# Kernel tuning notes

Hardware: AMD Instinct MI355X
Metric: run time of the kernel (lower is better)

The kernel has to match this reference:

```python
import jax, jax.numpy as jnp
import numpy as np

NUM_EMBEDDINGS = 1024
EMBEDDING_DIM = 256
COMMITMENT_COST = 0.25
DECAY = 0.99
EPS = 1e-05
BATCH = 65536


def setup_inputs() -> dict:
    key = jax.random.key(0)
    k1, k2 = jax.random.split(key, 2)
    z_e = jax.random.normal(k1, (BATCH, EMBEDDING_DIM), dtype=jnp.float32)
    embedding = jax.random.normal(k2, (NUM_EMBEDDINGS, EMBEDDING_DIM), dtype=jnp.float32)
    ema_cluster_size = jnp.zeros((NUM_EMBEDDINGS,), dtype=jnp.float32)
    ema_w = embedding  # buffer initialized as a clone of the codebook
    return {"z_e": z_e, "embedding": embedding,
            "ema_cluster_size": ema_cluster_size, "ema_w": ema_w}


def reference(z_e, embedding, ema_cluster_size, ema_w):
    B, D = z_e.shape
    K = embedding.shape[0]

    # Squared L2 distances: ||z||^2 + ||e||^2 - 2 z.e  -> [B, K]
    z_sq = jnp.sum(z_e * z_e, axis=1, keepdims=True)          # [B, 1]
    e_sq = jnp.sum(embedding * embedding, axis=1)[None, :]    # [1, K]
    ze = jnp.matmul(z_e, embedding.T)                         # [B, K]
    distances = z_sq + e_sq - 2.0 * ze

    encoding_indices = jnp.argmin(distances, axis=1)          # [B]

    # Gather instead of one-hot matmul (same math as encodings @ embedding)
    z_q = embedding[encoding_indices]                         # [B, D]
    z_q_st = z_e + jax.lax.stop_gradient(z_q - z_e)

    vq_loss = COMMITMENT_COST * jnp.mean(
        (jax.lax.stop_gradient(z_q) - z_e) ** 2)

    # EMA statistics (training-mode update); segment_sum == one-hot reductions
    cluster_size = jax.ops.segment_sum(
        jnp.ones((B,), dtype=z_e.dtype), encoding_indices, num_segments=K)
    new_ema_cluster_size = DECAY * ema_cluster_size + (1.0 - DECAY) * cluster_size
    dw = jax.ops.segment_sum(z_e, encoding_indices, num_segments=K)  # [K, D]
    new_ema_w = DECAY * ema_w + (1.0 - DECAY) * dw

    n = jnp.sum(new_ema_cluster_size)
    smoothed = (new_ema_cluster_size + EPS) / (n + K * EPS) * n
    new_embedding = new_ema_w / smoothed[:, None]

    avg_probs = cluster_size / B
    perplexity = jnp.exp(-jnp.sum(avg_probs * jnp.log(avg_probs + 1e-10)))

    return (z_q_st, vq_loss, perplexity, encoding_indices,
            new_embedding, new_ema_cluster_size, new_ema_w)
```

## Files before the change

### kernel.cpp

```cpp
#include <hip/hip_runtime.h>
#include <hip/hip_bf16.h>
#include <math.h>

#define BATCH 65536
#define DIM 256
#define KC 1024
#define COMMIT 0.25f
#define DECAY 0.99f
#define EPSV 1e-5f

#define O_ZQ   0
#define O_LOSS 16777216
#define O_PERP 16777217
#define O_IDX  16777218
#define O_EMB  16842754
#define O_NCS  17104898
#define O_NEW  17105922

typedef __attribute__((ext_vector_type(8))) short bf16x8;
typedef __attribute__((ext_vector_type(4))) float f32x4;

typedef __attribute__((address_space(1))) const void* as1_cvp;
typedef __attribute__((address_space(3))) void* as3_vp;

__device__ __forceinline__ void gload_lds16(const void* g, void* l) {
    __builtin_amdgcn_global_load_lds((as1_cvp)g, (as3_vp)l, 16, 0, 0);
}

__device__ __forceinline__ unsigned short bf16_rne(float x) {
    unsigned u = __builtin_bit_cast(unsigned, x);
    unsigned r = (u + 0x7FFFu + ((u >> 16) & 1u)) >> 16;
    return (unsigned short)r;
}
__device__ __forceinline__ float bf16_to_f(unsigned short h) {
    unsigned u = ((unsigned)h) << 16;
    return __builtin_bit_cast(float, u);
}

__global__ __launch_bounds__(256) void prep_zero_kernel(
        const float* __restrict__ emb,
        unsigned short* __restrict__ ehi, unsigned short* __restrict__ elo,
        float* __restrict__ e_sq, float* __restrict__ dw,
        int* __restrict__ counts, float* __restrict__ loss_part) {
    int k = blockIdx.x;
    int t = threadIdx.x;
    dw[(size_t)k * DIM + t] = 0.0f;
    if (t == 64) counts[k] = 0;
    if (k < 2 && t >= 128) loss_part[k * 128 + (t - 128)] = 0.0f;
    if (t < 64) {
        int lane = t;
        const float4* ep = (const float4*)(emb + (size_t)k * DIM);
        float4 e = ep[lane];
        float x[4] = {e.x, e.y, e.z, e.w};
        unsigned h[4], l[4];
        float s = 0.0f;
        #pragma unroll
        for (int j = 0; j < 4; ++j) {
            h[j] = bf16_rne(x[j]);
            l[j] = bf16_rne(x[j] - bf16_to_f((unsigned short)h[j]));
            s += x[j] * x[j];
        }
        uint2 ph = make_uint2(h[0] | (h[1] << 16), h[2] | (h[3] << 16));
        uint2 pl = make_uint2(l[0] | (l[1] << 16), l[2] | (l[3] << 16));
        int slot = lane >> 1;
        int half = lane & 1;
        int us = k * 256 + ((slot ^ (k & 7)) << 3) + (half << 2);
        *(uint2*)(ehi + us) = ph;
        *(uint2*)(elo + us) = pl;
        for (int off = 32; off; off >>= 1) s += __shfl_down(s, off, 64);
        if (lane == 0) e_sq[k] = s;
    }
}

#define CH_ROWS 32
__global__ __launch_bounds__(256, 2) void argmin_kernel(
        const float* __restrict__ z_e,
        const unsigned short* __restrict__ ehi,
        const unsigned short* __restrict__ elo,
        const float* __restrict__ e_sq,
        int* __restrict__ idx_out, float* __restrict__ idx_f_out,
        int* __restrict__ counts) {
    __shared__ __align__(16) unsigned short bhi_s[2][CH_ROWS * 256];
    __shared__ __align__(16) unsigned short blo_s[2][CH_ROWS * 256];
    __shared__ float esq_s[KC];

    int tid = threadIdx.x;
    int w = tid >> 6;
    int lane = tid & 63;
    int m16 = lane & 15;
    int quad = lane >> 4;
    int base_m = blockIdx.x * 128 + w * 32;

#define STAGE(c, b) { \
    const char* gh_ = (const char*)ehi + (c) * 16384 + tid * 16; \
    const char* gl_ = (const char*)elo + (c) * 16384 + tid * 16; \
    char* lh_ = (char*)(bhi_s[b]) + tid * 16; \
    char* ll_ = (char*)(blo_s[b]) + tid * 16; \
    _Pragma("unroll") for (int r_ = 0; r_ < 4; ++r_) { \
        gload_lds16(gh_ + r_ * 4096, lh_ + r_ * 4096); \
        gload_lds16(gl_ + r_ * 4096, ll_ + r_ * 4096); } }

    STAGE(0, 0)

    #pragma unroll
    for (int i = 0; i < 4; ++i) esq_s[tid + i * 256] = e_sq[tid + i * 256];

    bf16x8 ahi[2][8], alo[2][8];
    #pragma unroll
    for (int f = 0; f < 2; ++f) {
        const float* zr = z_e + (size_t)(base_m + f * 16 + m16) * DIM;
        #pragma unroll
        for (int ks = 0; ks < 8; ++ks) {
            const float4* p = (const float4*)(zr + ks * 32 + quad * 8);
            float4 x0 = p[0], x1 = p[1];
            float xs[8] = {x0.x, x0.y, x0.z, x0.w, x1.x, x1.y, x1.z, x1.w};
            #pragma unroll
            for (int j = 0; j < 8; ++j) {
                unsigned short h = bf16_rne(xs[j]);
                unsigned short l = bf16_rne(xs[j] - bf16_to_f(h));
                ahi[f][ks][j] = (short)h;
                alo[f][ks][j] = (short)l;
            }
        }
    }

    float best0[4] = {1e30f, 1e30f, 1e30f, 1e30f};
    float best1[4] = {1e30f, 1e30f, 1e30f, 1e30f};
    int bk0[4] = {0, 0, 0, 0};
    int bk1[4] = {0, 0, 0, 0};

    const int rsw = (m16 & 7) << 3;

#define COMPUTE(c, b) { \
    _Pragma("unroll") for (int f_ = 0; f_ < 2; ++f_) { \
        f32x4 acc0 = {0.f, 0.f, 0.f, 0.f}; \
        f32x4 acc1 = {0.f, 0.f, 0.f, 0.f}; \
        const unsigned short* bh_row = bhi_s[b] + (f_ * 16 + m16) * 256; \
        const unsigned short* bl_row = blo_s[b] + (f_ * 16 + m16) * 256; \
        _Pragma("unroll") for (int ks_ = 0; ks_ < 8; ++ks_) { \
            int us_off = (((ks_ * 4 + quad) << 3) ^ rsw); \
            bf16x8 bh = *(const bf16x8*)(bh_row + us_off); \
            bf16x8 bl = *(const bf16x8*)(bl_row + us_off); \
            acc0 = __builtin_amdgcn_mfma_f32_16x16x32_bf16(ahi[0][ks_], bh, acc0, 0, 0, 0); \
            acc1 = __builtin_amdgcn_mfma_f32_16x16x32_bf16(ahi[1][ks_], bh, acc1, 0, 0, 0); \
            acc0 = __builtin_amdgcn_mfma_f32_16x16x32_bf16(ahi[0][ks_], bl, acc0, 0, 0, 0); \
            acc1 = __builtin_amdgcn_mfma_f32_16x16x32_bf16(ahi[1][ks_], bl, acc1, 0, 0, 0); \
            acc0 = __builtin_amdgcn_mfma_f32_16x16x32_bf16(alo[0][ks_], bh, acc0, 0, 0, 0); \
            acc1 = __builtin_amdgcn_mfma_f32_16x16x32_bf16(alo[1][ks_], bh, acc1, 0, 0, 0); } \
        int col = (c) * 32 + f_ * 16 + m16; \
        float es = esq_s[col]; \
        _Pragma("unroll") for (int r_ = 0; r_ < 4; ++r_) { \
            float d0 = es - 2.0f * acc0[r_]; \
            float d1 = es - 2.0f * acc1[r_]; \
            if (d0 < best0[r_]) { best0[r_] = d0; bk0[r_] = col; } \
            if (d1 < best1[r_]) { best1[r_] = d1; bk1[r_] = col; } } } }

    __syncthreads();

    for (int c = 0; c < 32; c += 2) {
        STAGE(c + 1, 1)
        COMPUTE(c, 0)
        __syncthreads();
        if (c + 2 < 32) STAGE(c + 2, 0)
        COMPUTE(c + 1, 1)
        __syncthreads();
    }

    #pragma unroll
    for (int off = 1; off < 16; off <<= 1) {
        #pragma unroll
        for (int r = 0; r < 4; ++r) {
            float ov0 = __shfl_xor(best0[r], off, 64);
            int   ok0 = __shfl_xor(bk0[r], off, 64);
            if (ov0 < best0[r] || (ov0 == best0[r] && ok0 < bk0[r])) { best0[r] = ov0; bk0[r] = ok0; }
            float ov1 = __shfl_xor(best1[r], off, 64);
            int   ok1 = __shfl_xor(bk1[r], off, 64);
            if (ov1 < best1[r] || (ov1 == best1[r] && ok1 < bk1[r])) { best1[r] = ov1; bk1[r] = ok1; }
        }
    }
    if (m16 == 0) {
        #pragma unroll
        for (int r = 0; r < 4; ++r) {
            int row0 = base_m + quad * 4 + r;
            int row1 = base_m + 16 + quad * 4 + r;
            idx_out[row0] = bk0[r];
            idx_f_out[row0] = (float)bk0[r];
            idx_out[row1] = bk1[r];
            idx_f_out[row1] = (float)bk1[r];
            atomicAdd(&counts[bk0[r]], 1);
            atomicAdd(&counts[bk1[r]], 1);
        }
    }
#undef STAGE
#undef COMPUTE
}

__global__ __launch_bounds__(1024) void prefix_kernel(const int* __restrict__ counts,
                                                      int* __restrict__ cursor) {
    __shared__ int wsum[16];
    int t = threadIdx.x;
    int lane = t & 63;
    int wv = t >> 6;
    int c = counts[t];
    int x = c;
    #pragma unroll
    for (int off = 1; off < 64; off <<= 1) {
        int v = __shfl_up(x, off, 64);
        if (lane >= off) x += v;
    }
    if (lane == 63) wsum[wv] = x;
    __syncthreads();
    if (wv == 0) {
        int v = (lane < 16) ? wsum[lane] : 0;
        #pragma unroll
        for (int off = 1; off < 16; off <<= 1) {
            int u = __shfl_up(v, off, 64);
            if (lane >= off) v += u;
        }
        if (lane < 16) wsum[lane] = v;
    }
    __syncthreads();
    int woff = (wv == 0) ? 0 : wsum[wv - 1];
    cursor[t] = woff + x - c;
}

__global__ __launch_bounds__(256) void scatter_rows_kernel(
        const int* __restrict__ idx, int* __restrict__ cursor,
        int* __restrict__ sorted_rows) {
    int i = blockIdx.x * 256 + threadIdx.x;
    int k = idx[i];
    int pos = atomicAdd(&cursor[k], 1);
    sorted_rows[pos] = i;
}

#define SEG 64
__global__ __launch_bounds__(256) void dw_zq_kernel(
        const float* __restrict__ z_e, const float* __restrict__ emb,
        const int* __restrict__ idx, const int* __restrict__ sorted_rows,
        float* __restrict__ zq_out, float* __restrict__ dw,
        float* __restrict__ loss_part) {
    __shared__ int rows_s[SEG];
    __shared__ int keys_s[SEG];
    int t = threadIdx.x;
    int w = t >> 6;
    int lane = t & 63;
    int base = blockIdx.x * SEG;
    if (t < SEG) {
        int r = sorted_rows[base + t];
        rows_s[t] = r;
        keys_s[t] = idx[r];
    }
    __syncthreads();

    int c4 = lane * 4;
    float4 acc = make_float4(0.f, 0.f, 0.f, 0.f);
    float lsum = 0.0f;
    int kprev = keys_s[w * 16];
    #pragma unroll
    for (int g = 0; g < 2; ++g) {
        int rowb[8], kb[8];
        float4 zb[8], qb[8];
        #pragma unroll
        for (int u = 0; u < 8; ++u) {
            int i = w * 16 + g * 8 + u;
            rowb[u] = rows_s[i];
            kb[u] = keys_s[i];
        }
        #pragma unroll
        for (int u = 0; u < 8; ++u) {
            zb[u] = *(const float4*)(z_e + (size_t)rowb[u] * DIM + c4);
            qb[u] = *(const float4*)(emb + (size_t)kb[u] * DIM + c4);
        }
        #pragma unroll
        for (int u = 0; u < 8; ++u) {
            float4 z = zb[u], q = qb[u];
            float4 d = make_float4(q.x - z.x, q.y - z.y, q.z - z.z, q.w - z.w);
            float4 o = make_float4(z.x + d.x, z.y + d.y, z.z + d.z, z.w + d.w);
            *(float4*)(zq_out + (size_t)rowb[u] * DIM + c4) = o;
            lsum += d.x * d.x + d.y * d.y + d.z * d.z + d.w * d.w;
            if (kb[u] != kprev) {
                float* dst = dw + (size_t)kprev * DIM + c4;
                atomicAdd(dst + 0, acc.x);
                atomicAdd(dst + 1, acc.y);
                atomicAdd(dst + 2, acc.z);
                atomicAdd(dst + 3, acc.w);
                acc = make_float4(0.f, 0.f, 0.f, 0.f);
                kprev = kb[u];
            }
            acc.x += z.x; acc.y += z.y; acc.z += z.z; acc.w += z.w;
        }
    }
    {
        float* dst = dw + (size_t)kprev * DIM + c4;
        atomicAdd(dst + 0, acc.x);
        atomicAdd(dst + 1, acc.y);
        atomicAdd(dst + 2, acc.z);
        atomicAdd(dst + 3, acc.w);
    }

    __shared__ float red[256];
    red[t] = lsum;
    __syncthreads();
    for (int s = 128; s; s >>= 1) {
        if (t < s) red[t] += red[t + s];
        __syncthreads();
    }
    if (t == 0) atomicAdd(&loss_part[blockIdx.x & 255], red[0]);
}

__global__ __launch_bounds__(1024) void finalize_cluster(
        const float* __restrict__ ema_cs, const int* __restrict__ counts,
        const float* __restrict__ loss_part, float* __restrict__ out,
        float* __restrict__ n_ws) {
    __shared__ float s1[1024];
    __shared__ float s2[1024];
    __shared__ float s3[1024];
    int t = threadIdx.x;
    float c = (float)counts[t];
    float ncs = DECAY * ema_cs[t] + (1.0f - DECAY) * c;
    out[O_NCS + t] = ncs;
    float p = c / (float)BATCH;
    s1[t] = ncs;
    s2[t] = p * logf(p + 1e-10f);
    s3[t] = (t < 256) ? loss_part[t] : 0.0f;
    __syncthreads();
    for (int s = 512; s; s >>= 1) {
        if (t < s) { s1[t] += s1[t + s]; s2[t] += s2[t + s]; s3[t] += s3[t + s]; }
        __syncthreads();
    }
    if (t == 0) {
        n_ws[0] = s1[0];
        out[O_PERP] = expf(-s2[0]);
        out[O_LOSS] = COMMIT * s3[0] / (float)((size_t)BATCH * DIM);
    }
}

__global__ __launch_bounds__(256) void finalize_emb(
        const float* __restrict__ ema_w, const float* __restrict__ dw,
        const float* __restrict__ ncs_arr, const float* __restrict__ n_ws,
        float* __restrict__ out_emb, float* __restrict__ out_emaw) {
    int k = blockIdx.x;
    int d = threadIdx.x;
    size_t i = (size_t)k * DIM + d;
    float w = DECAY * ema_w[i] + (1.0f - DECAY) * dw[i];
    out_emaw[i] = w;
    float n = n_ws[0];
    float ncs = ncs_arr[k];
    float smoothed = (ncs + EPSV) / (n + (float)KC * EPSV) * n;
    out_emb[i] = w / smoothed;
}

extern "C" void kernel_launch(void* const* d_in, const int* in_sizes, int n_in,
                              void* d_out, int out_size, void* d_ws, size_t ws_size,
                              hipStream_t stream) {
    const float* z_e    = (const float*)d_in[0];
    const float* emb    = (const float*)d_in[1];
    const float* ema_cs = (const float*)d_in[2];
    const float* ema_w  = (const float*)d_in[3];
    float* out = (float*)d_out;
    float* ws = (float*)d_ws;

    float* dw            = ws;
    unsigned short* ehi  = (unsigned short*)(dw + KC * DIM);
    unsigned short* elo  = ehi + KC * DIM;
    float* e_sq          = (float*)(elo + KC * DIM);
    int* idx             = (int*)(e_sq + KC);
    int* counts          = idx + BATCH;
    int* cursor          = counts + KC;
    int* sorted_rows     = cursor + KC;
    float* loss_part     = (float*)(sorted_rows + BATCH);
    float* n_ws          = loss_part + 256;

    prep_zero_kernel<<<dim3(KC), dim3(256), 0, stream>>>(
        emb, ehi, elo, e_sq, dw, counts, loss_part);
    argmin_kernel<<<dim3(BATCH / 128), dim3(256), 0, stream>>>(
        z_e, ehi, elo, e_sq, idx, out + O_IDX, counts);
    prefix_kernel<<<dim3(1), dim3(1024), 0, stream>>>(counts, cursor);
    scatter_rows_kernel<<<dim3(BATCH / 256), dim3(256), 0, stream>>>(
        idx, cursor, sorted_rows);
    dw_zq_kernel<<<dim3(BATCH / SEG), dim3(256), 0, stream>>>(
        z_e, emb, idx, sorted_rows, out + O_ZQ, dw, loss_part);
    finalize_cluster<<<dim3(1), dim3(1024), 0, stream>>>(
        ema_cs, counts, loss_part, out, n_ws);
    finalize_emb<<<dim3(KC), dim3(256), 0, stream>>>(
        ema_w, dw, out + O_NCS, n_ws, out + O_EMB, out + O_NEW);
}
```

Before: 318.9 us.

## Halve argmin LDS chunk for higher occupancy and fold finalize kernels away

The argmin kernel now stages 16 codebook rows per chunk instead of 32, halving LDS use and raising launch bounds to 4 blocks per CU, with one 16-column tile per compute step. The cluster-size and perplexity stats move into the prefix kernel, and the loss is accumulated by a direct scaled atomicAdd into the output, removing the finalize_cluster launch. The smaller chunks mean more barriers and less reuse of the A fragments per LDS load. Going from 2 to 4 blocks per CU also tightens the register budget for the large ahi/alo fragment arrays, which risks spills.

Result: slower. 590.2 us (+85.1%).

```diff
diff --git a/kernel.cpp b/kernel.cpp
--- a/kernel.cpp
+++ b/kernel.cpp
@@ -41,12 +41,12 @@
         const float* __restrict__ emb,
         unsigned short* __restrict__ ehi, unsigned short* __restrict__ elo,
         float* __restrict__ e_sq, float* __restrict__ dw,
-        int* __restrict__ counts, float* __restrict__ loss_part) {
+        int* __restrict__ counts, float* __restrict__ out) {
     int k = blockIdx.x;
     int t = threadIdx.x;
     dw[(size_t)k * DIM + t] = 0.0f;
     if (t == 64) counts[k] = 0;
-    if (k < 2 && t >= 128) loss_part[k * 128 + (t - 128)] = 0.0f;
+    if (k == 0 && t == 128) out[O_LOSS] = 0.0f;
     if (t < 64) {
         int lane = t;
         const float4* ep = (const float4*)(emb + (size_t)k * DIM);
@@ -72,8 +72,8 @@
     }
 }
 
-#define CH_ROWS 32
-__global__ __launch_bounds__(256, 2) void argmin_kernel(
+#define CH_ROWS 16
+__global__ __launch_bounds__(256, 4) void argmin_kernel(
         const float* __restrict__ z_e,
         const unsigned short* __restrict__ ehi,
         const unsigned short* __restrict__ elo,
@@ -92,11 +92,11 @@
     int base_m = blockIdx.x * 128 + w * 32;
 
 #define STAGE(c, b) { \
-    const char* gh_ = (const char*)ehi + (c) * 16384 + tid * 16; \
-    const char* gl_ = (const char*)elo + (c) * 16384 + tid * 16; \
+    const char* gh_ = (const char*)ehi + (c) * 8192 + tid * 16; \
+    const char* gl_ = (const char*)elo + (c) * 8192 + tid * 16; \
     char* lh_ = (char*)(bhi_s[b]) + tid * 16; \
     char* ll_ = (char*)(blo_s[b]) + tid * 16; \
-    _Pragma("unroll") for (int r_ = 0; r_ < 4; ++r_) { \
+    _Pragma("unroll") for (int r_ = 0; r_ < 2; ++r_) { \
         gload_lds16(gh_ + r_ * 4096, lh_ + r_ * 4096); \
         gload_lds16(gl_ + r_ * 4096, ll_ + r_ * 4096); } }
 
@@ -132,36 +132,35 @@
     const int rsw = (m16 & 7) << 3;
 
 #define COMPUTE(c, b) { \
-    _Pragma("unroll") for (int f_ = 0; f_ < 2; ++f_) { \
-        f32x4 acc0 = {0.f, 0.f, 0.f, 0.f}; \
-        f32x4 acc1 = {0.f, 0.f, 0.f, 0.f}; \
-        const unsigned short* bh_row = bhi_s[b] + (f_ * 16 + m16) * 256; \
-        const unsigned short* bl_row = blo_s[b] + (f_ * 16 + m16) * 256; \
-        _Pragma("unroll") for (int ks_ = 0; ks_ < 8; ++ks_) { \
-            int us_off = (((ks_ * 4 + quad) << 3) ^ rsw); \
-            bf16x8 bh = *(const bf16x8*)(bh_row + us_off); \
-            bf16x8 bl = *(const bf16x8*)(bl_row + us_off); \
-            acc0 = __builtin_amdgcn_mfma_f32_16x16x32_bf16(ahi[0][ks_], bh, acc0, 0, 0, 0); \
-            acc1 = __builtin_amdgcn_mfma_f32_16x16x32_bf16(ahi[1][ks_], bh, acc1, 0, 0, 0); \
-            acc0 = __builtin_amdgcn_mfma_f32_16x16x32_bf16(ahi[0][ks_], bl, acc0, 0, 0, 0); \
-            acc1 = __builtin_amdgcn_mfma_f32_16x16x32_bf16(ahi[1][ks_], bl, acc1, 0, 0, 0); \
-            acc0 = __builtin_amdgcn_mfma_f32_16x16x32_bf16(alo[0][ks_], bh, acc0, 0, 0, 0); \
-            acc1 = __builtin_amdgcn_mfma_f32_16x16x32_bf16(alo[1][ks_], bh, acc1, 0, 0, 0); } \
-        int col = (c) * 32 + f_ * 16 + m16; \
-        float es = esq_s[col]; \
-        _Pragma("unroll") for (int r_ = 0; r_ < 4; ++r_) { \
-            float d0 = es - 2.0f * acc0[r_]; \
-            float d1 = es - 2.0f * acc1[r_]; \
-            if (d0 < best0[r_]) { best0[r_] = d0; bk0[r_] = col; } \
-            if (d1 < best1[r_]) { best1[r_] = d1; bk1[r_] = col; } } } }
-
-    __syncthreads();
-
-    for (int c = 0; c < 32; c += 2) {
+    f32x4 acc0 = {0.f, 0.f, 0.f, 0.f}; \
+    f32x4 acc1 = {0.f, 0.f, 0.f, 0.f}; \
+    const unsigned short* bh_row = bhi_s[b] + m16 * 256; \
+    const unsigned short* bl_row = blo_s[b] + m16 * 256; \
+    _Pragma("unroll") for (int ks_ = 0; ks_ < 8; ++ks_) { \
+        int us_off = (((ks_ * 4 + quad) << 3) ^ rsw); \
+        bf16x8 bh = *(const bf16x8*)(bh_row + us_off); \
+        bf16x8 bl = *(const bf16x8*)(bl_row + us_off); \
+        acc0 = __builtin_amdgcn_mfma_f32_16x16x32_bf16(ahi[0][ks_], bh, acc0, 0, 0, 0); \
+        acc1 = __builtin_amdgcn_mfma_f32_16x16x32_bf16(ahi[1][ks_], bh, acc1, 0, 0, 0); \
+        acc0 = __builtin_amdgcn_mfma_f32_16x16x32_bf16(ahi[0][ks_], bl, acc0, 0, 0, 0); \
+        acc1 = __builtin_amdgcn_mfma_f32_16x16x32_bf16(ahi[1][ks_], bl, acc1, 0, 0, 0); \
+        acc0 = __builtin_amdgcn_mfma_f32_16x16x32_bf16(alo[0][ks_], bh, acc0, 0, 0, 0); \
+        acc1 = __builtin_amdgcn_mfma_f32_16x16x32_bf16(alo[1][ks_], bh, acc1, 0, 0, 0); } \
+    int col = (c) * 16 + m16; \
+    float es = esq_s[col]; \
+    _Pragma("unroll") for (int r_ = 0; r_ < 4; ++r_) { \
+        float d0 = es - 2.0f * acc0[r_]; \
+        float d1 = es - 2.0f * acc1[r_]; \
+        if (d0 < best0[r_]) { best0[r_] = d0; bk0[r_] = col; } \
+        if (d1 < best1[r_]) { best1[r_] = d1; bk1[r_] = col; } } }
+
+    __syncthreads();
+
+    for (int c = 0; c < 64; c += 2) {
         STAGE(c + 1, 1)
         COMPUTE(c, 0)
         __syncthreads();
-        if (c + 2 < 32) STAGE(c + 2, 0)
+        if (c + 2 < 64) STAGE(c + 2, 0)
         COMPUTE(c + 1, 1)
         __syncthreads();
     }
@@ -195,9 +194,13 @@
 #undef COMPUTE
 }
 
-__global__ __launch_bounds__(1024) void prefix_kernel(const int* __restrict__ counts,
-                                                      int* __restrict__ cursor) {
+__global__ __launch_bounds__(1024) void prefix_stats_kernel(
+        const int* __restrict__ counts, int* __restrict__ cursor,
+        const float* __restrict__ ema_cs, float* __restrict__ out,
+        float* __restrict__ n_ws) {
     __shared__ int wsum[16];
+    __shared__ float s1[1024];
+    __shared__ float s2[1024];
     int t = threadIdx.x;
     int lane = t & 63;
     int wv = t >> 6;
@@ -209,6 +212,12 @@
         if (lane >= off) x += v;
     }
     if (lane == 63) wsum[wv] = x;
+    float cf = (float)c;
+    float ncs = DECAY * ema_cs[t] + (1.0f - DECAY) * cf;
+    out[O_NCS + t] = ncs;
+    float p = cf / (float)BATCH;
+    s1[t] = ncs;
+    s2[t] = p * logf(p + 1e-10f);
     __syncthreads();
     if (wv == 0) {
         int v = (lane < 16) ? wsum[lane] : 0;
@@ -222,6 +231,14 @@
     __syncthreads();
     int woff = (wv == 0) ? 0 : wsum[wv - 1];
     cursor[t] = woff + x - c;
+    for (int s = 512; s; s >>= 1) {
+        if (t < s) { s1[t] += s1[t + s]; s2[t] += s2[t + s]; }
+        __syncthreads();
+    }
+    if (t == 0) {
+        n_ws[0] = s1[0];
+        out[O_PERP] = expf(-s2[0]);
+    }
 }
 
 __global__ __launch_bounds__(256) void scatter_rows_kernel(
@@ -238,7 +255,7 @@
         const float* __restrict__ z_e, const float* __restrict__ emb,
         const int* __restrict__ idx, const int* __restrict__ sorted_rows,
         float* __restrict__ zq_out, float* __restrict__ dw,
-        float* __restrict__ loss_part) {
+        float* __restrict__ out) {
     __shared__ int rows_s[SEG];
     __shared__ int keys_s[SEG];
     int t = threadIdx.x;
@@ -305,34 +322,8 @@
         if (t < s) red[t] += red[t + s];
         __syncthreads();
     }
-    if (t == 0) atomicAdd(&loss_part[blockIdx.x & 255], red[0]);
-}
-
-__global__ __launch_bounds__(1024) void finalize_cluster(
-        const float* __restrict__ ema_cs, const int* __restrict__ counts,
-        const float* __restrict__ loss_part, float* __restrict__ out,
-        float* __restrict__ n_ws) {
-    __shared__ float s1[1024];
-    __shared__ float s2[1024];
-    __shared__ float s3[1024];
-    int t = threadIdx.x;
-    float c = (float)counts[t];
-    float ncs = DECAY * ema_cs[t] + (1.0f - DECAY) * c;
-    out[O_NCS + t] = ncs;
-    float p = c / (float)BATCH;
-    s1[t] = ncs;
-    s2[t] = p * logf(p + 1e-10f);
-    s3[t] = (t < 256) ? loss_part[t] : 0.0f;
-    __syncthreads();
-    for (int s = 512; s; s >>= 1) {
-        if (t < s) { s1[t] += s1[t + s]; s2[t] += s2[t + s]; s3[t] += s3[t + s]; }
-        __syncthreads();
-    }
-    if (t == 0) {
-        n_ws[0] = s1[0];
-        out[O_PERP] = expf(-s2[0]);
-        out[O_LOSS] = COMMIT * s3[0] / (float)((size_t)BATCH * DIM);
-    }
+    if (t == 0)
+        atomicAdd(out + O_LOSS, red[0] * (COMMIT / ((float)BATCH * (float)DIM)));
 }
 
 __global__ __launch_bounds__(256) void finalize_emb(
@@ -368,20 +359,18 @@
     int* counts          = idx + BATCH;
     int* cursor          = counts + KC;
     int* sorted_rows     = cursor + KC;
-    float* loss_part     = (float*)(sorted_rows + BATCH);
-    float* n_ws          = loss_part + 256;
+    float* n_ws          = (float*)(sorted_rows + BATCH);
 
     prep_zero_kernel<<<dim3(KC), dim3(256), 0, stream>>>(
-        emb, ehi, elo, e_sq, dw, counts, loss_part);
+        emb, ehi, elo, e_sq, dw, counts, out);
     argmin_kernel<<<dim3(BATCH / 128), dim3(256), 0, stream>>>(
         z_e, ehi, elo, e_sq, idx, out + O_IDX, counts);
-    prefix_kernel<<<dim3(1), dim3(1024), 0, stream>>>(counts, cursor);
+    prefix_stats_kernel<<<dim3(1), dim3(1024), 0, stream>>>(
+        counts, cursor, ema_cs, out, n_ws);
     scatter_rows_kernel<<<dim3(BATCH / 256), dim3(256), 0, stream>>>(
         idx, cursor, sorted_rows);
     dw_zq_kernel<<<dim3(BATCH / SEG), dim3(256), 0, stream>>>(
-        z_e, emb, idx, sorted_rows, out + O_ZQ, dw, loss_part);
-    finalize_cluster<<<dim3(1), dim3(1024), 0, stream>>>(
-        ema_cs, counts, loss_part, out, n_ws);
+        z_e, emb, idx, sorted_rows, out + O_ZQ, dw, out);
     finalize_emb<<<dim3(KC), dim3(256), 0, stream>>>(
         ema_w, dw, out + O_NCS, n_ws, out + O_EMB, out + O_NEW);
 }
```
